# Kernel tuning notes

Measured on AMD Instinct MI355X. Metric: run time of the kernel, lower is better.

Reference implementation:

```python
import jax, jax.numpy as jnp
import numpy as np

B, S, D, H = 4, 2048, 1024, 16
HD = D // H  # head_dim = 64


def setup_inputs() -> dict:
    key = jax.random.key(0)
    ks = jax.random.split(key, 5)
    scale = 0.02
    x = jax.random.normal(ks[0], (B, S, D), dtype=jnp.float32)
    Wq = jax.random.normal(ks[1], (D, D), dtype=jnp.float32) * scale
    Wk = jax.random.normal(ks[2], (D, D), dtype=jnp.float32) * scale
    Wv = jax.random.normal(ks[3], (D, D), dtype=jnp.float32) * scale
    Wo = jax.random.normal(ks[4], (D, D), dtype=jnp.float32) * scale
    # causal mask, broadcastable [1,1,S,S]; 0 entries get -10000 like masked_fill
    mask = jnp.tril(jnp.ones((S, S), dtype=jnp.int32))[None, None]
    return {"x": x, "Wq": Wq, "Wk": Wk, "Wv": Wv, "Wo": Wo, "mask": mask}


def reference(x, Wq, Wk, Wv, Wo, mask):
    b, s, _ = x.shape
    # nn.Linear: x @ W.T (no bias)
    q = (x @ Wq.T).reshape(b, s, H, HD).transpose(0, 2, 1, 3)  # [B,H,S,HD]
    k = (x @ Wk.T).reshape(b, s, H, HD).transpose(0, 2, 1, 3)
    v = (x @ Wv.T).reshape(b, s, H, HD).transpose(0, 2, 1, 3)
    attn = jnp.einsum('bhqd,bhkd->bhqk', q, k) / (HD ** 0.5)  # [B,H,S,S]
    attn = jnp.where(mask == 0, jnp.float32(-10000.0), attn)
    attn = jax.nn.softmax(attn, axis=-1)
    out = jnp.einsum('bhqk,bhkd->bhqd', attn, v)  # [B,H,S,HD]
    out = out.transpose(0, 2, 1, 3).reshape(b, s, H * HD)
    return out @ Wo.T
```

## Files before the change

kernel.cpp:

```cpp
#include <hip/hip_runtime.h>

typedef float    f4 __attribute__((ext_vector_type(4)));
typedef _Float16 h8 __attribute__((ext_vector_type(8)));
typedef _Float16 h4 __attribute__((ext_vector_type(4)));
typedef _Float16 h2 __attribute__((ext_vector_type(2)));
typedef unsigned u4 __attribute__((ext_vector_type(4)));

#define DEV static __device__ __forceinline__

DEV f4 mfma16(h8 a, h8 b, f4 c) {
  return __builtin_amdgcn_mfma_f32_16x16x32_f16(a, b, c, 0, 0, 0);
}

DEV void gload16(const void* g, void* lds) {
  __builtin_amdgcn_global_load_lds((__attribute__((address_space(1))) void*)g,
                                   (__attribute__((address_space(3))) void*)lds,
                                   16, 0, 0);
}

DEV unsigned cvtpku(float a, float b) {
  return __builtin_bit_cast(unsigned, __builtin_amdgcn_cvt_pkrtz(a, b));
}

DEV float max3f(float a, float b, float c) {
  float d;
  asm("v_max3_f32 %0, %1, %2, %3" : "=v"(d) : "v"(a), "v"(b), "v"(c));
  return d;
}

__global__ __launch_bounds__(256) void cvt_all(
    const float* __restrict__ x,  const float* __restrict__ wq,
    const float* __restrict__ wk, const float* __restrict__ wv,
    const float* __restrict__ wo,
    _Float16* __restrict__ xb, _Float16* __restrict__ wqkv, _Float16* __restrict__ wob)
{
  int b = blockIdx.x;
  const float* src; _Float16* dst; int i4;
  if      (b < 8192)  { src = x;  dst = xb;                 i4 = b * 256; }
  else if (b < 9216)  { src = wq; dst = wqkv;               i4 = (b - 8192)  * 256; }
  else if (b < 10240) { src = wk; dst = wqkv + (1u << 20);  i4 = (b - 9216)  * 256; }
  else if (b < 11264) { src = wv; dst = wqkv + (2u << 20);  i4 = (b - 10240) * 256; }
  else                { src = wo; dst = wob;                i4 = (b - 11264) * 256; }
  i4 += threadIdx.x;
  f4 v = ((const f4*)src)[i4];
  h4 o;
  o[0] = (_Float16)v[0]; o[1] = (_Float16)v[1];
  o[2] = (_Float16)v[2]; o[3] = (_Float16)v[3];
  ((h4*)dst)[i4] = o;
}

template<int MODE, int MF>
__global__ __launch_bounds__(512) void gemmT(
    const _Float16* __restrict__ A, const _Float16* __restrict__ Bt,
    float* __restrict__ C,
    _Float16* __restrict__ Qo, _Float16* __restrict__ Ko, _Float16* __restrict__ Vo,
    int N, int Nt)
{
  constexpr int ASZ = MF * 16 * 64;
  constexpr int BSZ = 8192;
  constexpr int V1  = (MF == 8) ? 12 : 9;
  constexpr int V2  = (MF == 8) ? 10 : 7;
  constexpr int VL3 = (MF == 8) ? 8 : 6;
  constexpr int VL5 = (MF == 8) ? 4 : 3;
  constexpr int VL6 = (MF == 8) ? 2 : 1;
  __shared__ _Float16 Al[4 * ASZ];
  __shared__ _Float16 Bl[4 * BSZ];

  int bid = blockIdx.x;
  int cpx = gridDim.x >> 3;
  bid = (bid & 7) * cpx + (bid >> 3);
  int tm = bid / Nt, tn = bid - tm * Nt;
  int m0 = tm * (MF * 32), n0 = tn * 256;

  int t = threadIdx.x, w = t >> 6, l = t & 63, lo = l & 15, hi = l >> 4;
  int wm = w >> 2, wn = w & 3;

  int rsc = t >> 3;
  int csrc = ((t & 7) ^ (rsc & 7)) * 8;
  const _Float16 *As[2][2], *Bs[2][2];
  #pragma unroll
  for (int q = 0; q < 2; ++q) {
    if (MF == 8) {
      As[q][0] = A + (size_t)(m0 + q * 64 + rsc) * 1024 + csrc;
      As[q][1] = A + (size_t)(m0 + 128 + q * 64 + rsc) * 1024 + csrc;
    } else {
      As[q][0] = A + (size_t)(m0 + (t >> 8) * 64 + q * 32 + (rsc & 31)) * 1024 + csrc;
      As[q][1] = As[q][0];
    }
    #pragma unroll
    for (int h = 0; h < 2; ++h)
      Bs[q][h] = Bt + (size_t)(n0 + (2 * h + (t >> 8)) * 64 + q * 32 + (rsc & 31)) * 1024 + csrc;
  }
  _Float16* Adst = Al + w * 512;
  _Float16* Bdst = Bl + w * 512;

  int awoff = wm * (MF * 8 * 64) + lo * 64;
  int bwoff = wn * 2048 + lo * 64;
  int s0 = (hi ^ (lo & 7)) * 8;
  int s1 = ((4 + hi) ^ (lo & 7)) * 8;

  f4 acc[MF][4] = {};
  h8 ar[MF / 2][2], br[2][2][2];

#define VMW(n)  asm volatile("s_waitcnt vmcnt(%0)" :: "n"(n) : "memory")
#define BARR    __builtin_amdgcn_s_barrier()
#define LGKM0   do { asm volatile("s_waitcnt lgkmcnt(0)" ::: "memory"); \
                     __builtin_amdgcn_sched_barrier(0); } while (0)
#define STA(BUF, Q, KO) do { \
    gload16(As[Q][0] + (KO), Adst + ((BUF) * 2 + (Q)) * ASZ); \
    if (MF == 8) gload16(As[Q][1] + (KO), Adst + ((BUF) * 2 + (Q)) * ASZ + 4096); \
  } while (0)
#define STB(BUF, QN, KO) do { \
    gload16(Bs[QN][0] + (KO), Bdst + ((BUF) * 2 + (QN)) * BSZ); \
    gload16(Bs[QN][1] + (KO), Bdst + ((BUF) * 2 + (QN)) * BSZ + 4096); \
  } while (0)
#define RDA(BUF, Q) do { \
    const _Float16* p_ = Al + ((BUF) * 2 + (Q)) * ASZ + awoff; \
    _Pragma("unroll") \
    for (int f_ = 0; f_ < MF / 2; ++f_) { \
      ar[f_][0] = *(const h8*)(p_ + f_ * 1024 + s0); \
      ar[f_][1] = *(const h8*)(p_ + f_ * 1024 + s1); } \
  } while (0)
#define RDB(BUF, QN, D) do { \
    const _Float16* p_ = Bl + ((BUF) * 2 + (QN)) * BSZ + bwoff; \
    br[D][0][0] = *(const h8*)(p_ + s0);        br[D][0][1] = *(const h8*)(p_ + s1); \
    br[D][1][0] = *(const h8*)(p_ + 1024 + s0); br[D][1][1] = *(const h8*)(p_ + 1024 + s1); \
  } while (0)
#define MM(MH, D) do { \
    __builtin_amdgcn_s_setprio(1); \
    _Pragma("unroll") \
    for (int f_ = 0; f_ < MF / 2; ++f_) \
      _Pragma("unroll") \
      for (int g_ = 0; g_ < 2; ++g_) { \
        acc[(MH) * (MF / 2) + f_][(D) * 2 + g_] = \
            mfma16(ar[f_][0], br[D][g_][0], acc[(MH) * (MF / 2) + f_][(D) * 2 + g_]); \
        acc[(MH) * (MF / 2) + f_][(D) * 2 + g_] = \
            mfma16(ar[f_][1], br[D][g_][1], acc[(MH) * (MF / 2) + f_][(D) * 2 + g_]); } \
    __builtin_amdgcn_s_setprio(0); \
    __builtin_amdgcn_sched_barrier(0); \
  } while (0)

  STA(0, 0, 0);  STB(0, 0, 0);  STB(0, 1, 0);  STA(0, 1, 0);
  STA(1, 0, 64); STB(1, 0, 64); STB(1, 1, 64); STA(1, 1, 64);

  int kof = 128;
  #pragma unroll 1
  for (int it = 0; it < 7; ++it) {
    VMW(V1); BARR; RDA(0, 0); RDB(0, 0, 0); LGKM0; MM(0, 0);
    VMW(V2); BARR; RDB(0, 1, 1); STA(0, 0, kof); STB(0, 0, kof); LGKM0; MM(0, 1);
    VMW(V1); BARR; RDA(0, 1); STB(0, 1, kof); LGKM0; MM(1, 1);
    BARR; STA(0, 1, kof); MM(1, 0);
    VMW(V1); BARR; RDA(1, 0); RDB(1, 0, 0); LGKM0; MM(0, 0);
    VMW(V2); BARR; RDB(1, 1, 1); STA(1, 0, kof + 64); STB(1, 0, kof + 64); LGKM0; MM(0, 1);
    VMW(V1); BARR; RDA(1, 1); STB(1, 1, kof + 64); LGKM0; MM(1, 1);
    BARR; STA(1, 1, kof + 64); MM(1, 0);
    kof += 128;
  }
  VMW(V1);  BARR; RDA(0, 0); RDB(0, 0, 0); LGKM0; MM(0, 0);
  VMW(V2);  BARR; RDB(0, 1, 1); LGKM0; MM(0, 1);
  VMW(VL3); BARR; RDA(0, 1); LGKM0; MM(1, 1);
  BARR; MM(1, 0);
  VMW(VL5); BARR; RDA(1, 0); RDB(1, 0, 0); LGKM0; MM(0, 0);
  VMW(VL6); BARR; RDB(1, 1, 1); LGKM0; MM(0, 1);
  VMW(0);   BARR; RDA(1, 1); LGKM0; MM(1, 1);
  BARR; MM(1, 0);

#undef VMW
#undef BARR
#undef LGKM0
#undef STA
#undef STB
#undef RDA
#undef RDB
#undef MM

  if (MODE == 0) {
    #pragma unroll
    for (int mi = 0; mi < MF; ++mi)
      #pragma unroll
      for (int nf = 0; nf < 4; ++nf)
        #pragma unroll
        for (int j = 0; j < 4; ++j) {
          int row = m0 + wm * (MF * 16) + mi * 16 + hi * 4 + j;
          int col = n0 + wn * 64 + nf * 16 + lo;
          C[(size_t)row * N + col] = acc[mi][nf][j];
        }
  } else {
    int which = n0 >> 10;
    int cb0 = (n0 & 1023) + wn * 64;
    if (which == 2) {
      #pragma unroll
      for (int mi = 0; mi < MF; ++mi) {
        int row0 = m0 + wm * (MF * 16) + mi * 16 + hi * 4;
        int bb = row0 >> 11, ss0 = row0 & 2047;
        #pragma unroll
        for (int nf = 0; nf < 4; ++nf) {
          int col = cb0 + nf * 16 + lo;
          int hh = col >> 6, hd = col & 63;
          h4 o4;
          o4[0] = (_Float16)acc[mi][nf][0]; o4[1] = (_Float16)acc[mi][nf][1];
          o4[2] = (_Float16)acc[mi][nf][2]; o4[3] = (_Float16)acc[mi][nf][3];
          *(h4*)(Vo + (size_t)(bb * 16 + hh) * 131072 + (size_t)hd * 2048 + ss0) = o4;
        }
      }
    } else {
      _Float16* Dst = (which == 0) ? Qo : Ko;
      float qs = (which == 0) ? 0.1803368801111137f : 1.0f;
      #pragma unroll
      for (int mi = 0; mi < MF; ++mi)
        #pragma unroll
        for (int nf = 0; nf < 4; ++nf)
          #pragma unroll
          for (int j = 0; j < 4; ++j) {
            int row = m0 + wm * (MF * 16) + mi * 16 + hi * 4 + j;
            int col = cb0 + nf * 16 + lo;
            int hh = col >> 6, hd = col & 63;
            int bb = row >> 11, ss = row & 2047;
            Dst[(size_t)(bb * 16 + hh) * 131072 + (size_t)ss * 64 + hd] =
                (_Float16)(acc[mi][nf][j] * qs);
          }
    }
  }
}

__global__ __launch_bounds__(512, 4) void attn_kernel(
    const _Float16* __restrict__ Q, const _Float16* __restrict__ Kb,
    const _Float16* __restrict__ Vb, _Float16* __restrict__ O)
{
  __shared__ _Float16 Kl[2 * 4096];
  __shared__ _Float16 Vl[2 * 4096];

  int bid = blockIdx.x;
  int bh = bid & 63, qi = 15 - (bid >> 6);
  int t = threadIdx.x, w = t >> 6, l = t & 63, lo = l & 15, hi = l >> 4;
  const size_t hoff = (size_t)bh * 131072;
  const _Float16* Kg = Kb + hoff;
  const _Float16* Vg = Vb + hoff;
  int bb = bh >> 4, hh = bh & 15;

  int rs = t >> 3, cs = t & 7;
  int sw_ = (cs ^ (rs & 7)) * 8;
  int sigma = ((rs & 0x1C) << 1) | (rs & 3) | ((rs & 32) >> 3);
  int srcK = sigma * 64 + sw_;
  int srcV = rs * 2048 + sw_;
  _Float16* kd0 = Kl + w * 512;
  _Float16* vd0 = Vl + w * 512;

  int koff[4][2];
  #pragma unroll
  for (int kf = 0; kf < 4; ++kf) {
    int row = kf * 16 + lo;
    koff[kf][0] = row * 64 + ((hi       ^ (row & 7)) * 8);
    koff[kf][1] = row * 64 + (((4 + hi) ^ (row & 7)) * 8);
  }

  h8 ones;
  #pragma unroll
  for (int e = 0; e < 8; ++e) ones[e] = (_Float16)1.0f;

  int qb = qi * 128 + w * 16;
  const _Float16* Qp = Q + hoff + (size_t)(qb + lo) * 64 + hi * 8;
  h8 qf0 = *(const h8*)(Qp);
  h8 qf1 = *(const h8*)(Qp + 32);

  f4 acc[4] = {};
  float m_run = -1e30f, l_run = 0.f;
  int nkt = 2 * qi + 2;

#define STAGE(buf, kt) do {                                                   \
    const _Float16* Kt_ = Kg + (size_t)(kt) * 4096;                           \
    const _Float16* Vt_ = Vg + (size_t)(kt) * 64;                             \
    gload16(Kt_ + srcK, kd0 + (buf) * 4096);                                  \
    gload16(Vt_ + srcV, vd0 + (buf) * 4096);                                  \
  } while (0)

#define ITER(kt, buf) do {                                                    \
    if ((kt) + 1 < nkt) STAGE(buf ^ 1, (kt) + 1);                             \
    const _Float16* Kc = Kl + (buf) * 4096;                                   \
    const _Float16* Vc = Vl + (buf) * 4096;                                   \
    f4 sc[4] = {};                                                            \
    __builtin_amdgcn_s_setprio(1);                                            \
    _Pragma("unroll")                                                         \
    for (int kf = 0; kf < 4; ++kf) {                                          \
      h8 k0 = *(const h8*)(Kc + koff[kf][0]);                                 \
      h8 k1 = *(const h8*)(Kc + koff[kf][1]);                                 \
      sc[kf] = mfma16(k0, qf0, sc[kf]);                                       \
      sc[kf] = mfma16(k1, qf1, sc[kf]);                                       \
    }                                                                         \
    __builtin_amdgcn_s_setprio(0);                                            \
    if ((kt) >= 2 * qi) {                                                     \
      int qg = qb + lo;                                                       \
      _Pragma("unroll")                                                       \
      for (int kf = 0; kf < 4; ++kf) {                                        \
        int kgb = (kt) * 64 + ((kf & 1) << 5) + ((kf >> 1) << 2) + hi * 8;    \
        _Pragma("unroll")                                                     \
        for (int j = 0; j < 4; ++j)                                           \
          if (kgb + j > qg) sc[kf][j] = -1e30f;                               \
      }                                                                       \
    }                                                                         \
    {                                                                         \
      f4 m4;                                                                  \
      _Pragma("unroll")                                                       \
      for (int c = 0; c < 4; ++c)                                             \
        m4[c] = fmaxf(max3f(sc[0][c], sc[1][c], sc[2][c]), sc[3][c]);         \
      float mx = fmaxf(max3f(m4[0], m4[1], m4[2]), m4[3]);                    \
      if (!__all(mx <= m_run + 8.f)) {              \
        mx = fmaxf(mx, __shfl_xor(mx, 16));                                   \
        mx = fmaxf(mx, __shfl_xor(mx, 32));                                   \
        float mn = fmaxf(m_run, mx);                                          \
        float cr = exp2f(m_run - mn);                                         \
        m_run = mn;                                                           \
        l_run *= cr;                                                          \
        _Pragma("unroll")                                                     \
        for (int df = 0; df < 4; ++df) {                                      \
          acc[df][0] *= cr; acc[df][1] *= cr;                                 \
          acc[df][2] *= cr; acc[df][3] *= cr;                                 \
        }                                                                     \
      }                                                                       \
    }                                                                         \
    f4 ls = {};                                                               \
    _Pragma("unroll")                                                         \
    for (int ks = 0; ks < 2; ++ks) {                                          \
      u4 tw;                                                                  \
      tw[0] = cvtpku(exp2f(sc[ks    ][0] - m_run),                            \
                     exp2f(sc[ks    ][1] - m_run));                           \
      tw[1] = cvtpku(exp2f(sc[ks    ][2] - m_run),                            \
                     exp2f(sc[ks    ][3] - m_run));                           \
      tw[2] = cvtpku(exp2f(sc[2 + ks][0] - m_run),                            \
                     exp2f(sc[2 + ks][1] - m_run));                           \
      tw[3] = cvtpku(exp2f(sc[2 + ks][2] - m_run),                            \
                     exp2f(sc[2 + ks][3] - m_run));                           \
      h8 pf = __builtin_bit_cast(h8, tw);                                     \
      ls = mfma16(ones, pf, ls);                                              \
      __builtin_amdgcn_s_setprio(1);                                          \
      _Pragma("unroll")                                                       \
      for (int df = 0; df < 4; ++df) {                                        \
        h8 vf = *(const h8*)(Vc + koff[df][ks]);                              \
        acc[df] = mfma16(vf, pf, acc[df]);                                    \
      }                                                                       \
      __builtin_amdgcn_s_setprio(0);                                          \
    }                                                                         \
    l_run += ls[0];                                                           \
    asm volatile("s_waitcnt vmcnt(0)" ::: "memory");                          \
    __syncthreads();                                                          \
  } while (0)

  STAGE(0, 0);
  asm volatile("s_waitcnt vmcnt(0)" ::: "memory");
  __syncthreads();

  for (int kt = 0; kt < nkt; kt += 2) {
    ITER(kt, 0);
    ITER(kt + 1, 1);
  }

  {
    float inv = 1.0f / l_run;
    int q = qb + lo;
    _Float16* Op = O + ((size_t)(bb * 2048 + q)) * 1024 + hh * 64 + (hi << 2);
    #pragma unroll
    for (int df = 0; df < 4; ++df) {
      h4 o4;
      o4[0] = (_Float16)(acc[df][0] * inv);
      o4[1] = (_Float16)(acc[df][1] * inv);
      o4[2] = (_Float16)(acc[df][2] * inv);
      o4[3] = (_Float16)(acc[df][3] * inv);
      *(h4*)(Op + df * 16) = o4;
    }
  }
#undef ITER
#undef STAGE
}

extern "C" void kernel_launch(void* const* d_in, const int* in_sizes, int n_in,
                              void* d_out, int out_size, void* d_ws, size_t ws_size,
                              hipStream_t stream)
{
  const float* x  = (const float*)d_in[0];
  const float* wq = (const float*)d_in[1];
  const float* wk = (const float*)d_in[2];
  const float* wv = (const float*)d_in[3];
  const float* wo = (const float*)d_in[4];

  char* ws = (char*)d_ws;
  _Float16* xb   = (_Float16*)(ws);
  _Float16* wqkv = (_Float16*)(ws + (16u << 20));
  _Float16* wob  = (_Float16*)(ws + (22u << 20));
  _Float16* Qb   = (_Float16*)(ws + (24u << 20));
  _Float16* Kb   = (_Float16*)(ws + (40u << 20));
  _Float16* Vb   = (_Float16*)(ws + (56u << 20));
  _Float16* Ob   = xb;

  cvt_all<<<12288, 256, 0, stream>>>(x, wq, wk, wv, wo, xb, wqkv, wob);
  gemmT<1, 8><<<32 * 12, 512, 0, stream>>>(xb, wqkv, nullptr, Qb, Kb, Vb, 3072, 12);
  attn_kernel<<<1024, 512, 0, stream>>>(Qb, Kb, Vb, Ob);
  gemmT<0, 4><<<64 * 4, 512, 0, stream>>>(Ob, wob, (float*)d_out,
                                          nullptr, nullptr, nullptr, 1024, 4);
}
```

Baseline: 163.0 us.

## Halve attention query tile to 64 rows with 256-thread blocks

The attention kernel now processes 64 query rows per block with 4 waves instead of 128 rows with 8 waves. The grid doubles to 2048 blocks and the loop becomes a single rolled loop with masking only on the final diagonal tile. Each thread now issues two global-to-LDS loads per tensor per stage so the same 64-key K/V tile is staged by half as many threads. The QKV GEMM is also switched to a smaller M tile with twice as many blocks. The aim is finer-grained load balance over the causal triangle and more concurrent blocks, at the cost of twice as many K/V tile loads from global memory per head and dropping the unrolled two-tile loop.

```diff
diff --git a/kernel.cpp b/kernel.cpp
--- a/kernel.cpp
+++ b/kernel.cpp
@@ -223,7 +223,7 @@
   }
 }
 
-__global__ __launch_bounds__(512, 4) void attn_kernel(
+__global__ __launch_bounds__(256) void attn_kernel(
     const _Float16* __restrict__ Q, const _Float16* __restrict__ Kb,
     const _Float16* __restrict__ Vb, _Float16* __restrict__ O)
 {
@@ -231,7 +231,7 @@
   __shared__ _Float16 Vl[2 * 4096];
 
   int bid = blockIdx.x;
-  int bh = bid & 63, qi = 15 - (bid >> 6);
+  int bh = bid & 63, qi = 31 - (bid >> 6);
   int t = threadIdx.x, w = t >> 6, l = t & 63, lo = l & 15, hi = l >> 4;
   const size_t hoff = (size_t)bh * 131072;
   const _Float16* Kg = Kb + hoff;
@@ -240,9 +240,9 @@
 
   int rs = t >> 3, cs = t & 7;
   int sw_ = (cs ^ (rs & 7)) * 8;
-  int sigma = ((rs & 0x1C) << 1) | (rs & 3) | ((rs & 32) >> 3);
-  int srcK = sigma * 64 + sw_;
-  int srcV = rs * 2048 + sw_;
+  int sigma = ((rs & 0x1C) << 1) | (rs & 3);
+  int srcK0 = sigma * 64 + sw_, srcK1 = srcK0 + 256;
+  int srcV0 = rs * 2048 + sw_,  srcV1 = srcV0 + 65536;
   _Float16* kd0 = Kl + w * 512;
   _Float16* vd0 = Vl + w * 512;
 
@@ -258,100 +258,104 @@
   #pragma unroll
   for (int e = 0; e < 8; ++e) ones[e] = (_Float16)1.0f;
 
-  int qb = qi * 128 + w * 16;
+  int qb = qi * 64 + w * 16;
   const _Float16* Qp = Q + hoff + (size_t)(qb + lo) * 64 + hi * 8;
   h8 qf0 = *(const h8*)(Qp);
   h8 qf1 = *(const h8*)(Qp + 32);
 
   f4 acc[4] = {};
   float m_run = -1e30f, l_run = 0.f;
-  int nkt = 2 * qi + 2;
+  int nkt = qi + 1;
 
 #define STAGE(buf, kt) do {                                                   \
     const _Float16* Kt_ = Kg + (size_t)(kt) * 4096;                           \
     const _Float16* Vt_ = Vg + (size_t)(kt) * 64;                             \
-    gload16(Kt_ + srcK, kd0 + (buf) * 4096);                                  \
-    gload16(Vt_ + srcV, vd0 + (buf) * 4096);                                  \
-  } while (0)
-
-#define ITER(kt, buf) do {                                                    \
-    if ((kt) + 1 < nkt) STAGE(buf ^ 1, (kt) + 1);                             \
-    const _Float16* Kc = Kl + (buf) * 4096;                                   \
-    const _Float16* Vc = Vl + (buf) * 4096;                                   \
-    f4 sc[4] = {};                                                            \
-    __builtin_amdgcn_s_setprio(1);                                            \
-    _Pragma("unroll")                                                         \
-    for (int kf = 0; kf < 4; ++kf) {                                          \
-      h8 k0 = *(const h8*)(Kc + koff[kf][0]);                                 \
-      h8 k1 = *(const h8*)(Kc + koff[kf][1]);                                 \
-      sc[kf] = mfma16(k0, qf0, sc[kf]);                                       \
-      sc[kf] = mfma16(k1, qf1, sc[kf]);                                       \
-    }                                                                         \
-    __builtin_amdgcn_s_setprio(0);                                            \
-    if ((kt) >= 2 * qi) {                                                     \
-      int qg = qb + lo;                                                       \
-      _Pragma("unroll")                                                       \
-      for (int kf = 0; kf < 4; ++kf) {                                        \
-        int kgb = (kt) * 64 + ((kf & 1) << 5) + ((kf >> 1) << 2) + hi * 8;    \
-        _Pragma("unroll")                                                     \
-        for (int j = 0; j < 4; ++j)                                           \
-          if (kgb + j > qg) sc[kf][j] = -1e30f;                               \
-      }                                                                       \
-    }                                                                         \
-    {                                                                         \
-      f4 m4;                                                                  \
-      _Pragma("unroll")                                                       \
-      for (int c = 0; c < 4; ++c)                                             \
-        m4[c] = fmaxf(max3f(sc[0][c], sc[1][c], sc[2][c]), sc[3][c]);         \
-      float mx = fmaxf(max3f(m4[0], m4[1], m4[2]), m4[3]);                    \
-      if (!__all(mx <= m_run + 8.f)) {              \
-        mx = fmaxf(mx, __shfl_xor(mx, 16));                                   \
-        mx = fmaxf(mx, __shfl_xor(mx, 32));                                   \
-        float mn = fmaxf(m_run, mx);                                          \
-        float cr = exp2f(m_run - mn);                                         \
-        m_run = mn;                                                           \
-        l_run *= cr;                                                          \
-        _Pragma("unroll")                                                     \
-        for (int df = 0; df < 4; ++df) {                                      \
-          acc[df][0] *= cr; acc[df][1] *= cr;                                 \
-          acc[df][2] *= cr; acc[df][3] *= cr;                                 \
-        }                                                                     \
-      }                                                                       \
-    }                                                                         \
-    f4 ls = {};                                                               \
-    _Pragma("unroll")                                                         \
-    for (int ks = 0; ks < 2; ++ks) {                                          \
-      u4 tw;                                                                  \
-      tw[0] = cvtpku(exp2f(sc[ks    ][0] - m_run),                            \
-                     exp2f(sc[ks    ][1] - m_run));                           \
-      tw[1] = cvtpku(exp2f(sc[ks    ][2] - m_run),                            \
-                     exp2f(sc[ks    ][3] - m_run));                           \
-      tw[2] = cvtpku(exp2f(sc[2 + ks][0] - m_run),                            \
-                     exp2f(sc[2 + ks][1] - m_run));                           \
-      tw[3] = cvtpku(exp2f(sc[2 + ks][2] - m_run),                            \
-                     exp2f(sc[2 + ks][3] - m_run));                           \
-      h8 pf = __builtin_bit_cast(h8, tw);                                     \
-      ls = mfma16(ones, pf, ls);                                              \
-      __builtin_amdgcn_s_setprio(1);                                          \
-      _Pragma("unroll")                                                       \
-      for (int df = 0; df < 4; ++df) {                                        \
-        h8 vf = *(const h8*)(Vc + koff[df][ks]);                              \
-        acc[df] = mfma16(vf, pf, acc[df]);                                    \
-      }                                                                       \
-      __builtin_amdgcn_s_setprio(0);                                          \
-    }                                                                         \
-    l_run += ls[0];                                                           \
-    asm volatile("s_waitcnt vmcnt(0)" ::: "memory");                          \
-    __syncthreads();                                                          \
+    gload16(Kt_ + srcK0, kd0 + (buf) * 4096);                                 \
+    gload16(Kt_ + srcK1, kd0 + (buf) * 4096 + 2048);                          \
+    gload16(Vt_ + srcV0, vd0 + (buf) * 4096);                                 \
+    gload16(Vt_ + srcV1, vd0 + (buf) * 4096 + 2048);                          \
   } while (0)
 
   STAGE(0, 0);
   asm volatile("s_waitcnt vmcnt(0)" ::: "memory");
   __syncthreads();
 
-  for (int kt = 0; kt < nkt; kt += 2) {
-    ITER(kt, 0);
-    ITER(kt + 1, 1);
+  #pragma unroll 1
+  for (int kt = 0; kt < nkt; ++kt) {
+    int buf = kt & 1;
+    if (kt + 1 < nkt) STAGE(buf ^ 1, kt + 1);
+    const _Float16* Kc = Kl + buf * 4096;
+    const _Float16* Vc = Vl + buf * 4096;
+
+    f4 sc[4] = {};
+    __builtin_amdgcn_s_setprio(1);
+    #pragma unroll
+    for (int kf = 0; kf < 4; ++kf) {
+      h8 k0 = *(const h8*)(Kc + koff[kf][0]);
+      h8 k1 = *(const h8*)(Kc + koff[kf][1]);
+      sc[kf] = mfma16(k0, qf0, sc[kf]);
+      sc[kf] = mfma16(k1, qf1, sc[kf]);
+    }
+    __builtin_amdgcn_s_setprio(0);
+
+    if (kt == nkt - 1) {
+      int qg = qb + lo;
+      #pragma unroll
+      for (int kf = 0; kf < 4; ++kf) {
+        int kgb = kt * 64 + ((kf & 1) << 5) + ((kf >> 1) << 2) + hi * 8;
+        #pragma unroll
+        for (int j = 0; j < 4; ++j)
+          if (kgb + j > qg) sc[kf][j] = -1e30f;
+      }
+    }
+
+    {
+      f4 m4;
+      #pragma unroll
+      for (int c = 0; c < 4; ++c)
+        m4[c] = fmaxf(max3f(sc[0][c], sc[1][c], sc[2][c]), sc[3][c]);
+      float mx = fmaxf(max3f(m4[0], m4[1], m4[2]), m4[3]);
+      if (!__all(mx <= m_run + 8.f)) {
+        mx = fmaxf(mx, __shfl_xor(mx, 16));
+        mx = fmaxf(mx, __shfl_xor(mx, 32));
+        float mn = fmaxf(m_run, mx);
+        float cr = exp2f(m_run - mn);
+        m_run = mn;
+        l_run *= cr;
+        #pragma unroll
+        for (int df = 0; df < 4; ++df) {
+          acc[df][0] *= cr; acc[df][1] *= cr;
+          acc[df][2] *= cr; acc[df][3] *= cr;
+        }
+      }
+    }
+
+    f4 ls = {};
+    #pragma unroll
+    for (int ks = 0; ks < 2; ++ks) {
+      u4 tw;
+      tw[0] = cvtpku(exp2f(sc[ks    ][0] - m_run),
+                     exp2f(sc[ks    ][1] - m_run));
+      tw[1] = cvtpku(exp2f(sc[ks    ][2] - m_run),
+                     exp2f(sc[ks    ][3] - m_run));
+      tw[2] = cvtpku(exp2f(sc[2 + ks][0] - m_run),
+                     exp2f(sc[2 + ks][1] - m_run));
+      tw[3] = cvtpku(exp2f(sc[2 + ks][2] - m_run),
+                     exp2f(sc[2 + ks][3] - m_run));
+      h8 pf = __builtin_bit_cast(h8, tw);
+      ls = mfma16(ones, pf, ls);
+      __builtin_amdgcn_s_setprio(1);
+      #pragma unroll
+      for (int df = 0; df < 4; ++df) {
+        h8 vf = *(const h8*)(Vc + koff[df][ks]);
+        acc[df] = mfma16(vf, pf, acc[df]);
+      }
+      __builtin_amdgcn_s_setprio(0);
+    }
+    l_run += ls[0];
+
+    asm volatile("s_waitcnt vmcnt(0)" ::: "memory");
+    __syncthreads();
   }
 
   {
@@ -368,7 +372,6 @@
       *(h4*)(Op + df * 16) = o4;
     }
   }
-#undef ITER
 #undef STAGE
 }
 
@@ -392,8 +395,8 @@
   _Float16* Ob   = xb;
 
   cvt_all<<<12288, 256, 0, stream>>>(x, wq, wk, wv, wo, xb, wqkv, wob);
-  gemmT<1, 8><<<32 * 12, 512, 0, stream>>>(xb, wqkv, nullptr, Qb, Kb, Vb, 3072, 12);
-  attn_kernel<<<1024, 512, 0, stream>>>(Qb, Kb, Vb, Ob);
+  gemmT<1, 4><<<64 * 12, 512, 0, stream>>>(xb, wqkv, nullptr, Qb, Kb, Vb, 3072, 12);
+  attn_kernel<<<2048, 256, 0, stream>>>(Qb, Kb, Vb, Ob);
   gemmT<0, 4><<<64 * 4, 512, 0, stream>>>(Ob, wob, (float*)d_out,
                                           nullptr, nullptr, nullptr, 1024, 4);
 }
```

Measured after the change: 173.0 us. 1.06x slower.
